# Kernel optimization log

Hardware: AMD Instinct MI355X
Metric: run time of the kernel (lower is better)

The kernel has to match this reference:

```python
import jax, jax.numpy as jnp
import numpy as np

L_XYZ = 10  # fourier freqs for position -> 3 + 6*10 = 63 dims
L_DIR = 4   # fourier freqs for direction -> 3 + 6*4 = 27 dims
DIM = 32    # radiance feature dim per depth layer
PPP = 4     # points (depth layers) per pixel
HID = 128   # MLP hidden width
UCH = 64    # UNet hidden channels


def pe(x, L):
    # fourier positional encoding: [x, sin(2^k x), cos(2^k x)]
    f = (2.0 ** jnp.arange(L)).astype(x.dtype)
    xf = x[..., None] * f  # [..., 3, L]
    s = jnp.sin(xf).reshape(x.shape[:-1] + (-1,))
    c = jnp.cos(xf).reshape(x.shape[:-1] + (-1,))
    return jnp.concatenate([x, s, c], axis=-1)


def conv(x, w, b):
    y = jax.lax.conv_general_dilated(x, w, (1, 1), 'SAME',
                                     dimension_numbers=('NCHW', 'OIHW', 'NCHW'))
    return y + b[None, :, None, None]


def setup_inputs() -> dict:
    key = jax.random.key(0)
    ks = jax.random.split(key, 24)
    H = W = 384
    zbufs = jax.random.uniform(ks[0], (H, W, PPP), dtype=jnp.float32)  # depths in [0,1)
    o = jax.random.normal(ks[1], (H, W, 3), dtype=jnp.float32)
    d = jax.random.normal(ks[2], (H, W, 3), dtype=jnp.float32)
    d = d / jnp.linalg.norm(d, axis=-1, keepdims=True)
    cos = jax.random.uniform(ks[3], (H, W, 1), dtype=jnp.float32) * 0.5 + 0.5
    ray = jnp.concatenate([o, d, cos], axis=-1)  # [H,W,7]
    gt = jax.random.uniform(ks[4], (H, W, 3), dtype=jnp.float32)
    mask_gt = jnp.ones((H, W, 1), dtype=jnp.float32)
    xyz_o = jax.random.normal(ks[5], (1024, 3), dtype=jnp.float32)
    in_xyz = 3 + 6 * L_XYZ
    in_dir = 3 + 6 * L_DIR
    in_ch = DIM * PPP
    p = {}
    p['w1'] = jax.random.normal(ks[6], (in_xyz, HID), dtype=jnp.float32) * 0.05
    p['b1'] = jnp.zeros((HID,), dtype=jnp.float32)
    p['w2'] = jax.random.normal(ks[7], (HID, HID), dtype=jnp.float32) * 0.05
    p['b2'] = jnp.zeros((HID,), dtype=jnp.float32)
    p['w3'] = jax.random.normal(ks[8], (HID + in_dir, DIM), dtype=jnp.float32) * 0.05
    p['b3'] = jnp.zeros((DIM,), dtype=jnp.float32)
    p['mpn_w1'] = jax.random.normal(ks[9], (in_ch, in_ch, 3, 3), dtype=jnp.float32) * 0.02
    p['mpn_b1'] = jnp.zeros((in_ch,), dtype=jnp.float32)
    p['mpn_w2'] = jax.random.normal(ks[10], (in_ch, in_ch, 3, 3), dtype=jnp.float32) * 0.02
    p['mpn_b2'] = jnp.zeros((in_ch,), dtype=jnp.float32)
    p['uw1'] = jax.random.normal(ks[11], (UCH, in_ch, 3, 3), dtype=jnp.float32) * 0.02
    p['ub1'] = jnp.zeros((UCH,), dtype=jnp.float32)
    p['uw2'] = jax.random.normal(ks[12], (UCH, UCH, 3, 3), dtype=jnp.float32) * 0.02
    p['ub2'] = jnp.zeros((UCH,), dtype=jnp.float32)
    p['uw3'] = jax.random.normal(ks[13], (3, UCH, 3, 3), dtype=jnp.float32) * 0.02
    p['ub3'] = jnp.zeros((3,), dtype=jnp.float32)
    inp = {'zbufs': zbufs, 'ray': ray, 'gt': gt, 'mask_gt': mask_gt,
           'isTrain': 1, 'xyz_o': xyz_o}
    inp.update(p)
    return inp


def reference(zbufs, ray, gt, mask_gt, isTrain, xyz_o,
              w1, b1, w2, b2, w3, b3,
              mpn_w1, mpn_b1, mpn_w2, mpn_b2,
              uw1, ub1, uw2, ub2, uw3, ub3):
    H, W, P = zbufs.shape
    o = ray[..., :3]
    dirs = ray[..., 3:6]
    cos = ray[..., 6:7]
    thresh = 0.2 if isTrain else 0.0
    # dense equivalent of boolean-mask gather -> MLP -> scatter into zeros
    mask = (zbufs > thresh).astype(zbufs.dtype)  # [H,W,P]
    # xyz_near = o + dirs * zbuf / cos  (xyznear path)
    xyz = o[..., None, :] + dirs[..., None, :] * zbufs[..., None] / cos[..., None]  # [H,W,P,3]
    x = pe(xyz, L_XYZ)                                   # [H,W,P,63]
    h = jax.nn.relu(x @ w1 + b1)                         # [H,W,P,HID]
    h = jax.nn.relu(h @ w2 + b2)
    dpe = pe(dirs, L_DIR)                                # [H,W,27]
    dpe = jnp.broadcast_to(dpe[..., None, :], h.shape[:-1] + (dpe.shape[-1],))
    feat = jnp.concatenate([h, dpe], axis=-1) @ w3 + b3  # [H,W,P,DIM]
    feat = feat * mask[..., None]                        # zeros where pix_mask is False
    # per-layer permute(2,3,0,1) + cat(dim=1) == [1, P*DIM, H, W]
    rdmp = feat.transpose(2, 3, 0, 1).reshape(1, P * DIM, H, W)
    # MPN: predicted per-channel mask
    m = jax.nn.sigmoid(conv(jax.nn.relu(conv(rdmp, mpn_w1, mpn_b1)), mpn_w2, mpn_b2))
    fuse = rdmp * m
    fea_map = jax.nn.sigmoid(fuse[0, :3].transpose(1, 2, 0))  # [H,W,3]
    # UNet refinement to RGB
    u = jax.nn.relu(conv(fuse, uw1, ub1))
    u = jax.nn.relu(conv(u, uw2, ub2))
    img = jax.nn.sigmoid(conv(u, uw3, ub3))[0].transpose(1, 2, 0)  # [H,W,3]
    return img
```

## Files before the change

kernel.cpp:

```cpp
#include <hip/hip_runtime.h>
#include <hip/hip_bf16.h>
#include <math.h>

typedef __attribute__((ext_vector_type(8))) unsigned short ushort8;
typedef __attribute__((ext_vector_type(8))) __bf16 bf16x8;
typedef __attribute__((ext_vector_type(4))) float floatx4;

constexpr int IMGW = 384;
constexpr int NPIX = IMGW * IMGW;

__device__ __forceinline__ unsigned short f2bf(float f) {
  union { float f; unsigned u; } v; v.f = f;
  unsigned u = v.u;
  return (unsigned short)((u + 0x7fffu + ((u >> 16) & 1u)) >> 16);
}
__device__ __forceinline__ float bf2f(unsigned short h) {
  union { unsigned u; float f; } v; v.u = ((unsigned)h) << 16; return v.f;
}
__device__ __forceinline__ unsigned pk2bf(float a, float b) {
  float2 f2; f2.x = a; f2.y = b;
  __hip_bfloat162 h = __float22bfloat162_rn(f2);
  union { __hip_bfloat162 h; unsigned u; } u; u.h = h; return u.u;
}
__device__ __forceinline__ floatx4 mfma16(bf16x8 a, bf16x8 b, floatx4 c) {
  return __builtin_amdgcn_mfma_f32_16x16x32_bf16(a, b, c, 0, 0, 0);
}
__device__ __forceinline__ bf16x8 lds_frag(const unsigned short* p) {
  return *reinterpret_cast<const bf16x8*>(p);
}
__device__ __forceinline__ bf16x8 u4_to_bf(uint4 v) {
  union { uint4 u; bf16x8 b; } c; c.u = v; return c.b;
}

__device__ __forceinline__ void convB_elem(const float* __restrict__ w,
                                           unsigned short* __restrict__ wt,
                                           int i, int CIN, int G, int NT) {
  int j = i & 7, lane = (i >> 3) & 63;
  int rest = i >> 9;
  int nt = rest % NT; int rest2 = rest / NT;
  int g = rest2 % G;  int ks = rest2 / G;
  int q = lane >> 4, m = lane & 15;
  int co = (g * NT + nt) * 16 + m;
  int k = ks * 32 + q * 8 + j;
  int nb = k / CIN, ci = k - nb * CIN;
  wt[i] = f2bf(w[(co * CIN + ci) * 9 + nb]);
}

__global__ __launch_bounds__(256) void prep_all(
    const float* __restrict__ w1, const float* __restrict__ w2, const float* __restrict__ w3,
    const float* __restrict__ mw1, const float* __restrict__ mw2,
    const float* __restrict__ uw1, const float* __restrict__ uw2,
    unsigned short* __restrict__ w1A, unsigned short* __restrict__ w2A,
    unsigned short* __restrict__ w3A,
    unsigned short* __restrict__ cw1, unsigned short* __restrict__ cw2,
    unsigned short* __restrict__ cu1, unsigned short* __restrict__ cu2) {
  int i = blockIdx.x * 256 + threadIdx.x;
  if (i < 28672) {
    if (i < 8192) {
      int j = i & 7, lane = (i >> 3) & 63, t = i >> 9;
      int mt = t >> 1, ks = t & 1;
      int ch_out = mt * 16 + (lane & 15);
      int kp = ks * 32 + (lane >> 4) * 8 + j;
      int chunk = kp >> 3, sl = kp & 7;
      float val;
      if (chunk == 7 && sl >= 4) {
        int c = sl - 4;
        val = (c < 3) ? w1[c * 128 + ch_out] : 0.0f;
      } else {
        const int coordA[8] = {0,0,0,1,1,2,2,2};
        const int octA[8]   = {0,4,8,2,6,0,4,8};
        const int coordB[8] = {0,0,1,1,1,2,2,2};
        const int octB[8]   = {2,6,0,4,8,2,6,0};
        int rc  = (sl < 4) ? coordA[chunk] : coordB[chunk];
        int oct = ((sl < 4) ? octA[chunk] : octB[chunk]) + ((sl >> 1) & 1);
        int korig = ((sl & 1) ? 33 : 3) + rc * 10 + oct;
        val = w1[korig * 128 + ch_out];
      }
      w1A[i] = f2bf(val);
    } else if (i < 24576) {
      int i2 = i - 8192;
      int j = i2 & 7, lane = (i2 >> 3) & 63, t = i2 >> 9;
      int mt = t >> 2, ks = t & 3;
      int ch_out = mt * 16 + (lane & 15);
      int kp = ks * 32 + (lane >> 4) * 8 + j;
      int c_orig = ((kp >> 2) & 7) * 16 + (kp >> 5) * 4 + (kp & 3);
      w2A[i2] = f2bf(w2[c_orig * 128 + ch_out]);
    } else {
      int i3 = i - 24576;
      int j = i3 & 7, lane = (i3 >> 3) & 63, t = i3 >> 9;
      int mt = t >> 2, ks = t & 3;
      int ch_out = mt * 16 + (lane & 15);
      int kp = ks * 32 + (lane >> 4) * 8 + j;
      int c_orig = ((kp >> 2) & 7) * 16 + (kp >> 5) * 4 + (kp & 3);
      w3A[i3] = f2bf(w3[c_orig * 32 + ch_out]);
    }
    return;
  }
  i -= 28672;
  if (i < 147456) { convB_elem(mw1, cw1, i, 128, 4, 2); return; }
  i -= 147456;
  if (i < 147456) { convB_elem(mw2, cw2, i, 128, 4, 2); return; }
  i -= 147456;
  if (i < 73728)  { convB_elem(uw1, cu1, i, 128, 4, 1); return; }
  i -= 73728;
  if (i < 36864)  { convB_elem(uw2, cu2, i, 64, 4, 1); return; }
}

__global__ __launch_bounds__(256) void dcon_kernel(
    const float* __restrict__ ray, const float* __restrict__ w3,
    const float* __restrict__ b3, float* __restrict__ dconG) {
  int gid = blockIdx.x * 256 + threadIdx.x;
  int pixel = gid >> 5, c = gid & 31;
  const float* r = ray + (size_t)pixel * 7;
  float d0 = r[3], d1 = r[4], d2 = r[5];
  float acc = b3[c];
  acc += d0 * w3[128 * 32 + c] + d1 * w3[129 * 32 + c] + d2 * w3[130 * 32 + c];
  float dv[3] = { d0, d1, d2 };
  #pragma unroll
  for (int cc = 0; cc < 3; ++cc) {
    float fs = 1.0f;
    #pragma unroll
    for (int f = 0; f < 4; ++f) {
      float s, co;
      __sincosf(dv[cc] * fs, &s, &co);
      acc += s * w3[(131 + cc * 4 + f) * 32 + c];
      acc += co * w3[(143 + cc * 4 + f) * 32 + c];
      fs *= 2.0f;
    }
  }
  dconG[gid] = acc;
}

__global__ __launch_bounds__(64, 3) void mlp_kernel(
    const float* __restrict__ zbufs, const float* __restrict__ ray,
    const int* __restrict__ isTrain,
    const float* __restrict__ b1, const float* __restrict__ b2,
    const unsigned short* __restrict__ w1A, const unsigned short* __restrict__ w2A,
    const unsigned short* __restrict__ w3A, const float* __restrict__ dconG,
    unsigned short* __restrict__ rdmp) {
  __shared__ __align__(16) unsigned short H[64 * 136];

  const int lane = threadIdx.x;
  const int q = lane >> 4, m = lane & 15;
  const float thresh = (isTrain[0] != 0) ? 0.2f : 0.0f;

  float fA[2], fB[2];
  int cAi[2], cBi[2];
  #pragma unroll
  for (int half = 0; half < 2; ++half) {
    int ch = half * 4 + q;
    cAi[half] = (ch <= 2) ? 0 : ((ch <= 4) ? 1 : 2);
    fA[half]  = (ch == 0 || ch == 5) ? 1.0f :
                (ch == 1 || ch == 6) ? 16.0f :
                (ch == 2 || ch == 7) ? 256.0f :
                (ch == 3) ? 4.0f : 64.0f;
    cBi[half] = (ch <= 1) ? 0 : ((ch <= 4) ? 1 : 2);
    fB[half]  = (ch == 2) ? 1.0f :
                (ch == 0 || ch == 5) ? 4.0f :
                (ch == 3) ? 16.0f :
                (ch == 1 || ch == 6) ? 64.0f : 256.0f;
  }

  bf16x8 bx[4][2];
  float zs[4];
  #pragma unroll
  for (int nt = 0; nt < 4; ++nt) {
    int s = nt * 16 + m;
    int sg = blockIdx.x * 64 + s;
    int pixel = sg >> 2;
    float z = zbufs[sg];
    zs[nt] = z;
    const float* r = ray + (size_t)pixel * 7;
    float t = z / r[6];
    float xv0 = r[0] + r[3] * t, xv1 = r[1] + r[4] * t, xv2 = r[2] + r[5] * t;
    #pragma unroll
    for (int half = 0; half < 2; ++half) {
      float uA = (cAi[half] == 0) ? xv0 : ((cAi[half] == 1) ? xv1 : xv2);
      float uB = (cBi[half] == 0) ? xv0 : ((cBi[half] == 1) ? xv1 : xv2);
      float sa, ca, sb, cb;
      __sincosf(uA * fA[half], &sa, &ca);
      __sincosf(uB * fB[half], &sb, &cb);
      float t2a = sa + sa;
      float sa1 = t2a * ca, ca1 = fmaf(-t2a, sa, 1.0f);
      float t2b = sb + sb;
      float sb1 = t2b * cb, cb1 = fmaf(-t2b, sb, 1.0f);
      if (half == 1 && q == 3) { sb = xv0; cb = xv1; sb1 = xv2; cb1 = 0.0f; }
      uint4 dv;
      dv.x = pk2bf(sa, ca); dv.y = pk2bf(sa1, ca1);
      dv.z = pk2bf(sb, cb); dv.w = pk2bf(sb1, cb1);
      bx[nt][half] = u4_to_bf(dv);
    }
  }

  #pragma unroll 1
  for (int half = 0; half < 2; ++half) {
    floatx4 acc[4][4];
    #pragma unroll
    for (int mt = 0; mt < 4; ++mt) {
      float4 bb = *reinterpret_cast<const float4*>(b1 + (half * 4 + mt) * 16 + q * 4);
      #pragma unroll
      for (int nt = 0; nt < 4; ++nt) {
        acc[mt][nt][0] = bb.x; acc[mt][nt][1] = bb.y;
        acc[mt][nt][2] = bb.z; acc[mt][nt][3] = bb.w;
      }
    }
    #pragma unroll
    for (int ks = 0; ks < 2; ++ks) {
      #pragma unroll
      for (int mt = 0; mt < 4; ++mt) {
        int mtg = half * 4 + mt;
        bf16x8 a = *reinterpret_cast<const bf16x8*>(w1A + (((mtg << 1) + ks) << 9) + lane * 8);
        #pragma unroll
        for (int nt = 0; nt < 4; ++nt)
          acc[mt][nt] = mfma16(a, bx[nt][ks], acc[mt][nt]);
      }
    }
    #pragma unroll
    for (int nt = 0; nt < 4; ++nt) {
      uint4* base = reinterpret_cast<uint4*>(&H[(nt * 16 + m) * 136 + q * 32 + half * 16]);
      #pragma unroll
      for (int g = 0; g < 2; ++g) {
        uint4 v;
        v.x = pk2bf(fmaxf(acc[2*g][nt][0], 0.0f),   fmaxf(acc[2*g][nt][1], 0.0f));
        v.y = pk2bf(fmaxf(acc[2*g][nt][2], 0.0f),   fmaxf(acc[2*g][nt][3], 0.0f));
        v.z = pk2bf(fmaxf(acc[2*g+1][nt][0], 0.0f), fmaxf(acc[2*g+1][nt][1], 0.0f));
        v.w = pk2bf(fmaxf(acc[2*g+1][nt][2], 0.0f), fmaxf(acc[2*g+1][nt][3], 0.0f));
        base[g] = v;
      }
    }
  }

  {
    uint4 keep[4][2];
    #pragma unroll 1
    for (int half = 0; half < 2; ++half) {
      floatx4 acc[4][4];
      #pragma unroll
      for (int mt = 0; mt < 4; ++mt) {
        float4 bb = *reinterpret_cast<const float4*>(b2 + (half * 4 + mt) * 16 + q * 4);
        #pragma unroll
        for (int nt = 0; nt < 4; ++nt) {
          acc[mt][nt][0] = bb.x; acc[mt][nt][1] = bb.y;
          acc[mt][nt][2] = bb.z; acc[mt][nt][3] = bb.w;
        }
      }
      #pragma unroll 1
      for (int ks = 0; ks < 4; ++ks) {
        bf16x8 bf[4];
        #pragma unroll
        for (int nt = 0; nt < 4; ++nt)
          bf[nt] = lds_frag(H + (nt * 16 + m) * 136 + ks * 32 + q * 8);
        #pragma unroll
        for (int mt = 0; mt < 4; ++mt) {
          int mtg = half * 4 + mt;
          bf16x8 a = *reinterpret_cast<const bf16x8*>(w2A + (((mtg << 2) + ks) << 9) + lane * 8);
          #pragma unroll
          for (int nt = 0; nt < 4; ++nt)
            acc[mt][nt] = mfma16(a, bf[nt], acc[mt][nt]);
        }
      }
      #pragma unroll
      for (int nt = 0; nt < 4; ++nt) {
        #pragma unroll
        for (int g = 0; g < 2; ++g) {
          uint4 v;
          v.x = pk2bf(fmaxf(acc[2*g][nt][0], 0.0f),   fmaxf(acc[2*g][nt][1], 0.0f));
          v.y = pk2bf(fmaxf(acc[2*g][nt][2], 0.0f),   fmaxf(acc[2*g][nt][3], 0.0f));
          v.z = pk2bf(fmaxf(acc[2*g+1][nt][0], 0.0f), fmaxf(acc[2*g+1][nt][1], 0.0f));
          v.w = pk2bf(fmaxf(acc[2*g+1][nt][2], 0.0f), fmaxf(acc[2*g+1][nt][3], 0.0f));
          if (half == 0) {
            keep[nt][g] = v;
          } else {
            *reinterpret_cast<uint4*>(&H[(nt * 16 + m) * 136 + q * 32 + 16 + g * 8]) = v;
          }
        }
      }
    }
    #pragma unroll
    for (int nt = 0; nt < 4; ++nt)
      #pragma unroll
      for (int g = 0; g < 2; ++g)
        *reinterpret_cast<uint4*>(&H[(nt * 16 + m) * 136 + q * 32 + g * 8]) = keep[nt][g];
  }

  {
    floatx4 acc[2][4];
    const float* dg = dconG + (size_t)blockIdx.x * 512;
    #pragma unroll
    for (int nt = 0; nt < 4; ++nt) {
      int s = nt * 16 + m;
      #pragma unroll
      for (int mt = 0; mt < 2; ++mt)
        acc[mt][nt] = *reinterpret_cast<const floatx4*>(dg + (s >> 2) * 32 + mt * 16 + q * 4);
    }
    #pragma unroll 2
    for (int ks = 0; ks < 4; ++ks) {
      bf16x8 bf[4];
      #pragma unroll
      for (int nt = 0; nt < 4; ++nt)
        bf[nt] = lds_frag(H + (nt * 16 + m) * 136 + ks * 32 + q * 8);
      #pragma unroll
      for (int mt = 0; mt < 2; ++mt) {
        bf16x8 a = *reinterpret_cast<const bf16x8*>(w3A + (((mt << 2) + ks) << 9) + lane * 8);
        #pragma unroll
        for (int nt = 0; nt < 4; ++nt)
          acc[mt][nt] = mfma16(a, bf[nt], acc[mt][nt]);
      }
    }
    #pragma unroll
    for (int nt = 0; nt < 4; ++nt) {
      int s = nt * 16 + m;
      float mk = (zs[nt] > thresh) ? 1.0f : 0.0f;
      unsigned short* dst = rdmp + (size_t)blockIdx.x * 2048 + s * 32 + q * 4;
      #pragma unroll
      for (int mt = 0; mt < 2; ++mt) {
        uint2 pk;
        pk.x = pk2bf(acc[mt][nt][0] * mk, acc[mt][nt][1] * mk);
        pk.y = pk2bf(acc[mt][nt][2] * mk, acc[mt][nt][3] * mk);
        *reinterpret_cast<uint2*>(dst + mt * 16) = pk;
      }
    }
  }
}

template<int CIN, int COUT, int MODE, int MINW>
__global__ __launch_bounds__(512, MINW) void conv3x3(
    const unsigned short* __restrict__ in, const unsigned short* __restrict__ wt,
    const float* __restrict__ bias, const unsigned short* __restrict__ rdmp,
    unsigned short* __restrict__ out) {
  constexpr int CP  = CIN + 8;
  constexpr int CH8 = CIN / 8;
  constexpr int KC  = CIN / 32;
  constexpr int NT  = COUT / 64;
  constexpr int GROUPS = KC * 3;
  __shared__ __align__(16) unsigned short lds_in[10 * 18 * CP];

  const int tid = threadIdx.x;
  const int x0 = blockIdx.x * 16, y0 = blockIdx.y * 8;

  for (int i = tid; i < 180 * CH8; i += 512) {
    int pix = i / CH8, part = i - pix * CH8;
    int xx = pix % 18, yy = pix / 18;
    int gx = x0 - 1 + xx, gy = y0 - 1 + yy;
    ushort8 v = {0, 0, 0, 0, 0, 0, 0, 0};
    if (gx >= 0 && gx < IMGW && gy >= 0 && gy < IMGW)
      v = *reinterpret_cast<const ushort8*>(in + ((size_t)(gy * IMGW + gx)) * CIN + part * 8);
    *reinterpret_cast<ushort8*>(&lds_in[pix * CP + part * 8]) = v;
  }
  __syncthreads();

  const int wave = tid >> 6, lane = tid & 63, q = lane >> 4, m = lane & 15;
  const int cw = wave & 3;
  const int rw = wave >> 2;
  floatx4 acc[4][NT] = {};

  auto loadB = [&](int g, bf16x8 (&bb)[3][NT]) {
    int kc = g / 3, dx = g - kc * 3;
    #pragma unroll
    for (int dy = 0; dy < 3; ++dy) {
      int ks = (dy * 3 + dx) * KC + kc;
      #pragma unroll
      for (int nt = 0; nt < NT; ++nt)
        bb[dy][nt] = *reinterpret_cast<const bf16x8*>(
            wt + ((((size_t)ks * 4 + cw) * NT + nt) << 9) + lane * 8);
    }
  };
  auto compute = [&](int g, bf16x8 (&bb)[3][NT]) {
    int kc = g / 3, dx = g - kc * 3;
    bf16x8 a[6];
    #pragma unroll
    for (int rr = 0; rr < 6; ++rr)
      a[rr] = lds_frag(&lds_in[((rw * 4 + rr) * 18 + m + dx) * CP + kc * 32 + q * 8]);
    #pragma unroll
    for (int dy = 0; dy < 3; ++dy)
      #pragma unroll
      for (int nt = 0; nt < NT; ++nt)
        #pragma unroll
        for (int mt = 0; mt < 4; ++mt)
          acc[mt][nt] = mfma16(a[mt + dy], bb[dy][nt], acc[mt][nt]);
  };

  bf16x8 b0[3][NT], b1[3][NT];
  loadB(0, b0);
  #pragma unroll 1
  for (int g = 0; g < GROUPS; g += 2) {
    loadB(g + 1, b1);
    compute(g, b0);
    if (g + 2 < GROUPS) loadB(g + 2, b0);
    compute(g + 1, b1);
  }

  const int co0 = cw * (COUT / 4);
  #pragma unroll
  for (int mt = 0; mt < 4; ++mt) {
    int y = y0 + rw * 4 + mt;
    #pragma unroll
    for (int nt = 0; nt < NT; ++nt) {
      int co = co0 + nt * 16 + m;
      float bb = bias[co];
      #pragma unroll
      for (int r = 0; r < 4; ++r) {
        int pixel = y * IMGW + x0 + q * 4 + r;
        float v = acc[mt][nt][r] + bb;
        if (MODE == 0) {
          v = fmaxf(v, 0.0f);
        } else {
          v = 1.0f / (1.0f + __expf(-v));
          v *= bf2f(rdmp[(size_t)pixel * 128 + co]);
        }
        out[(size_t)pixel * COUT + co] = f2bf(v);
      }
    }
  }
}

__global__ __launch_bounds__(256) void uconv3_kernel(
    const unsigned short* __restrict__ u2, const float* __restrict__ w,
    const float* __restrict__ b, float* __restrict__ out) {
  __shared__ float wl[1728];
  for (int i = threadIdx.x; i < 1728; i += 256) {
    int c = i % 3; int t = i / 3; int ci = t & 63; int nb = t >> 6;
    wl[i] = w[(c * 64 + ci) * 9 + nb];
  }
  __syncthreads();
  int pixel = blockIdx.x * 256 + threadIdx.x;
  int py = pixel / IMGW, px = pixel - py * IMGW;
  float a0 = b[0], a1 = b[1], a2 = b[2];
  for (int nb = 0; nb < 9; ++nb) {
    int gy = py + nb / 3 - 1, gx = px + nb % 3 - 1;
    if (gx < 0 || gx >= IMGW || gy < 0 || gy >= IMGW) continue;
    const unsigned short* src = u2 + (size_t)(gy * IMGW + gx) * 64;
    const float* wp = wl + nb * 192;
    #pragma unroll
    for (int cc = 0; cc < 8; ++cc) {
      ushort8 v = *reinterpret_cast<const ushort8*>(src + cc * 8);
      #pragma unroll
      for (int j = 0; j < 8; ++j) {
        float uv = bf2f(v[j]);
        const float* w3p = wp + (cc * 8 + j) * 3;
        a0 += uv * w3p[0]; a1 += uv * w3p[1]; a2 += uv * w3p[2];
      }
    }
  }
  float* o = out + (size_t)pixel * 3;
  o[0] = 1.0f / (1.0f + __expf(-a0));
  o[1] = 1.0f / (1.0f + __expf(-a1));
  o[2] = 1.0f / (1.0f + __expf(-a2));
}

extern "C" void kernel_launch(void* const* d_in, const int* in_sizes, int n_in,
                              void* d_out, int out_size, void* d_ws, size_t ws_size,
                              hipStream_t stream) {
  (void)in_sizes; (void)n_in; (void)out_size; (void)ws_size;
  const float* zbufs = (const float*)d_in[0];
  const float* ray   = (const float*)d_in[1];
  const int* isTrain = (const int*)d_in[4];
  const float* w1 = (const float*)d_in[6];
  const float* b1 = (const float*)d_in[7];
  const float* w2 = (const float*)d_in[8];
  const float* b2 = (const float*)d_in[9];
  const float* w3 = (const float*)d_in[10];
  const float* b3 = (const float*)d_in[11];
  const float* mpn_w1 = (const float*)d_in[12];
  const float* mpn_b1 = (const float*)d_in[13];
  const float* mpn_w2 = (const float*)d_in[14];
  const float* mpn_b2 = (const float*)d_in[15];
  const float* uw1 = (const float*)d_in[16];
  const float* ub1 = (const float*)d_in[17];
  const float* uw2 = (const float*)d_in[18];
  const float* ub2 = (const float*)d_in[19];
  const float* uw3 = (const float*)d_in[20];
  const float* ub3 = (const float*)d_in[21];
  float* out = (float*)d_out;

  unsigned char* ws = (unsigned char*)d_ws;
  size_t off = 0;
  auto alloc = [&](size_t bytes) -> void* {
    void* p = ws + off; off = (off + bytes + 255) & ~(size_t)255; return p;
  };
  unsigned short* w1A  = (unsigned short*)alloc(8192 * 2);
  unsigned short* w2A  = (unsigned short*)alloc(16384 * 2);
  unsigned short* w3A  = (unsigned short*)alloc(4096 * 2);
  unsigned short* cw1  = (unsigned short*)alloc((size_t)128 * 1152 * 2);
  unsigned short* cw2  = (unsigned short*)alloc((size_t)128 * 1152 * 2);
  unsigned short* cu1  = (unsigned short*)alloc((size_t)64 * 1152 * 2);
  unsigned short* cu2  = (unsigned short*)alloc((size_t)64 * 576 * 2);
  unsigned short* rdmp = (unsigned short*)alloc((size_t)NPIX * 128 * 2);
  unsigned short* t1   = (unsigned short*)alloc((size_t)NPIX * 128 * 2);
  unsigned short* fuse = (unsigned short*)alloc((size_t)NPIX * 128 * 2);
  unsigned short* u1 = t1;
  unsigned short* u2 = rdmp;
  float* dconG = (float*)fuse;

  prep_all<<<1696, 256, 0, stream>>>(w1, w2, w3, mpn_w1, mpn_w2, uw1, uw2,
                                     w1A, w2A, w3A, cw1, cw2, cu1, cu2);
  dcon_kernel<<<NPIX * 32 / 256, 256, 0, stream>>>(ray, w3, b3, dconG);
  mlp_kernel<<<NPIX * 4 / 64, 64, 0, stream>>>(zbufs, ray, isTrain, b1, b2,
                                               w1A, w2A, w3A, dconG, rdmp);

  dim3 cgrid(IMGW / 16, IMGW / 8);
  conv3x3<128, 128, 0, 4><<<cgrid, 512, 0, stream>>>(rdmp, cw1, mpn_b1, nullptr, t1);
  conv3x3<128, 128, 1, 4><<<cgrid, 512, 0, stream>>>(t1, cw2, mpn_b2, rdmp, fuse);
  conv3x3<128, 64, 0, 4><<<cgrid, 512, 0, stream>>>(fuse, cu1, ub1, nullptr, u1);
  conv3x3<64, 64, 0, 4><<<cgrid, 512, 0, stream>>>(u1, cu2, ub2, nullptr, u2);
  uconv3_kernel<<<NPIX / 256, 256, 0, stream>>>(u2, uw3, ub3, out);
}
```

Baseline: 337.3 us.

## Split MLP kernel output halves across two waves per block

The MLP kernel now launches 128 threads per block. Each of the two waves handles one half of the hidden/output channels for the same 64 samples, where before a single wave looped over both halves serially. Barriers are added around the shared hidden-activation buffer so layer-2 outputs are written only after both waves finish reading layer-1 results. This doubles the waves working on each sample tile and aims for more latency hiding. The cost is that both waves redundantly compute the positional encoding, and the extra barriers add synchronisation overhead.

```diff
diff --git a/kernel.cpp b/kernel.cpp
--- a/kernel.cpp
+++ b/kernel.cpp
@@ -131,7 +131,7 @@
   dconG[gid] = acc;
 }
 
-__global__ __launch_bounds__(64, 3) void mlp_kernel(
+__global__ __launch_bounds__(128, 4) void mlp_kernel(
     const float* __restrict__ zbufs, const float* __restrict__ ray,
     const int* __restrict__ isTrain,
     const float* __restrict__ b1, const float* __restrict__ b2,
@@ -140,25 +140,27 @@
     unsigned short* __restrict__ rdmp) {
   __shared__ __align__(16) unsigned short H[64 * 136];
 
-  const int lane = threadIdx.x;
+  const int tid = threadIdx.x;
+  const int half = tid >> 6;
+  const int lane = tid & 63;
   const int q = lane >> 4, m = lane & 15;
   const float thresh = (isTrain[0] != 0) ? 0.2f : 0.0f;
 
   float fA[2], fB[2];
   int cAi[2], cBi[2];
   #pragma unroll
-  for (int half = 0; half < 2; ++half) {
-    int ch = half * 4 + q;
-    cAi[half] = (ch <= 2) ? 0 : ((ch <= 4) ? 1 : 2);
-    fA[half]  = (ch == 0 || ch == 5) ? 1.0f :
-                (ch == 1 || ch == 6) ? 16.0f :
-                (ch == 2 || ch == 7) ? 256.0f :
-                (ch == 3) ? 4.0f : 64.0f;
-    cBi[half] = (ch <= 1) ? 0 : ((ch <= 4) ? 1 : 2);
-    fB[half]  = (ch == 2) ? 1.0f :
-                (ch == 0 || ch == 5) ? 4.0f :
-                (ch == 3) ? 16.0f :
-                (ch == 1 || ch == 6) ? 64.0f : 256.0f;
+  for (int ks = 0; ks < 2; ++ks) {
+    int ch = ks * 4 + q;
+    cAi[ks] = (ch <= 2) ? 0 : ((ch <= 4) ? 1 : 2);
+    fA[ks]  = (ch == 0 || ch == 5) ? 1.0f :
+              (ch == 1 || ch == 6) ? 16.0f :
+              (ch == 2 || ch == 7) ? 256.0f :
+              (ch == 3) ? 4.0f : 64.0f;
+    cBi[ks] = (ch <= 1) ? 0 : ((ch <= 4) ? 1 : 2);
+    fB[ks]  = (ch == 2) ? 1.0f :
+              (ch == 0 || ch == 5) ? 4.0f :
+              (ch == 3) ? 16.0f :
+              (ch == 1 || ch == 6) ? 64.0f : 256.0f;
   }
 
   bf16x8 bx[4][2];
@@ -174,26 +176,25 @@
     float t = z / r[6];
     float xv0 = r[0] + r[3] * t, xv1 = r[1] + r[4] * t, xv2 = r[2] + r[5] * t;
     #pragma unroll
-    for (int half = 0; half < 2; ++half) {
-      float uA = (cAi[half] == 0) ? xv0 : ((cAi[half] == 1) ? xv1 : xv2);
-      float uB = (cBi[half] == 0) ? xv0 : ((cBi[half] == 1) ? xv1 : xv2);
+    for (int ks = 0; ks < 2; ++ks) {
+      float uA = (cAi[ks] == 0) ? xv0 : ((cAi[ks] == 1) ? xv1 : xv2);
+      float uB = (cBi[ks] == 0) ? xv0 : ((cBi[ks] == 1) ? xv1 : xv2);
       float sa, ca, sb, cb;
-      __sincosf(uA * fA[half], &sa, &ca);
-      __sincosf(uB * fB[half], &sb, &cb);
+      __sincosf(uA * fA[ks], &sa, &ca);
+      __sincosf(uB * fB[ks], &sb, &cb);
       float t2a = sa + sa;
       float sa1 = t2a * ca, ca1 = fmaf(-t2a, sa, 1.0f);
       float t2b = sb + sb;
       float sb1 = t2b * cb, cb1 = fmaf(-t2b, sb, 1.0f);
-      if (half == 1 && q == 3) { sb = xv0; cb = xv1; sb1 = xv2; cb1 = 0.0f; }
+      if (ks == 1 && q == 3) { sb = xv0; cb = xv1; sb1 = xv2; cb1 = 0.0f; }
       uint4 dv;
       dv.x = pk2bf(sa, ca); dv.y = pk2bf(sa1, ca1);
       dv.z = pk2bf(sb, cb); dv.w = pk2bf(sb1, cb1);
-      bx[nt][half] = u4_to_bf(dv);
-    }
-  }
-
-  #pragma unroll 1
-  for (int half = 0; half < 2; ++half) {
+      bx[nt][ks] = u4_to_bf(dv);
+    }
+  }
+
+  {
     floatx4 acc[4][4];
     #pragma unroll
     for (int mt = 0; mt < 4; ++mt) {
@@ -229,11 +230,11 @@
       }
     }
   }
+  __syncthreads();
 
   {
     uint4 keep[4][2];
-    #pragma unroll 1
-    for (int half = 0; half < 2; ++half) {
+    {
       floatx4 acc[4][4];
       #pragma unroll
       for (int mt = 0; mt < 4; ++mt) {
@@ -268,30 +269,26 @@
           v.y = pk2bf(fmaxf(acc[2*g][nt][2], 0.0f),   fmaxf(acc[2*g][nt][3], 0.0f));
           v.z = pk2bf(fmaxf(acc[2*g+1][nt][0], 0.0f), fmaxf(acc[2*g+1][nt][1], 0.0f));
           v.w = pk2bf(fmaxf(acc[2*g+1][nt][2], 0.0f), fmaxf(acc[2*g+1][nt][3], 0.0f));
-          if (half == 0) {
-            keep[nt][g] = v;
-          } else {
-            *reinterpret_cast<uint4*>(&H[(nt * 16 + m) * 136 + q * 32 + 16 + g * 8]) = v;
-          }
+          keep[nt][g] = v;
         }
       }
     }
+    __syncthreads();
     #pragma unroll
     for (int nt = 0; nt < 4; ++nt)
       #pragma unroll
       for (int g = 0; g < 2; ++g)
-        *reinterpret_cast<uint4*>(&H[(nt * 16 + m) * 136 + q * 32 + g * 8]) = keep[nt][g];
-  }
+        *reinterpret_cast<uint4*>(&H[(nt * 16 + m) * 136 + q * 32 + half * 16 + g * 8]) = keep[nt][g];
+  }
+  __syncthreads();
 
   {
-    floatx4 acc[2][4];
+    floatx4 acc[4];
     const float* dg = dconG + (size_t)blockIdx.x * 512;
     #pragma unroll
     for (int nt = 0; nt < 4; ++nt) {
       int s = nt * 16 + m;
-      #pragma unroll
-      for (int mt = 0; mt < 2; ++mt)
-        acc[mt][nt] = *reinterpret_cast<const floatx4*>(dg + (s >> 2) * 32 + mt * 16 + q * 4);
+      acc[nt] = *reinterpret_cast<const floatx4*>(dg + (s >> 2) * 32 + half * 16 + q * 4);
     }
     #pragma unroll 2
     for (int ks = 0; ks < 4; ++ks) {
@@ -299,26 +296,20 @@
       #pragma unroll
       for (int nt = 0; nt < 4; ++nt)
         bf[nt] = lds_frag(H + (nt * 16 + m) * 136 + ks * 32 + q * 8);
-      #pragma unroll
-      for (int mt = 0; mt < 2; ++mt) {
-        bf16x8 a = *reinterpret_cast<const bf16x8*>(w3A + (((mt << 2) + ks) << 9) + lane * 8);
-        #pragma unroll
-        for (int nt = 0; nt < 4; ++nt)
-          acc[mt][nt] = mfma16(a, bf[nt], acc[mt][nt]);
-      }
+      bf16x8 a = *reinterpret_cast<const bf16x8*>(w3A + (((half << 2) + ks) << 9) + lane * 8);
+      #pragma unroll
+      for (int nt = 0; nt < 4; ++nt)
+        acc[nt] = mfma16(a, bf[nt], acc[nt]);
     }
     #pragma unroll
     for (int nt = 0; nt < 4; ++nt) {
       int s = nt * 16 + m;
       float mk = (zs[nt] > thresh) ? 1.0f : 0.0f;
-      unsigned short* dst = rdmp + (size_t)blockIdx.x * 2048 + s * 32 + q * 4;
-      #pragma unroll
-      for (int mt = 0; mt < 2; ++mt) {
-        uint2 pk;
-        pk.x = pk2bf(acc[mt][nt][0] * mk, acc[mt][nt][1] * mk);
-        pk.y = pk2bf(acc[mt][nt][2] * mk, acc[mt][nt][3] * mk);
-        *reinterpret_cast<uint2*>(dst + mt * 16) = pk;
-      }
+      unsigned short* dst = rdmp + (size_t)blockIdx.x * 2048 + s * 32 + q * 4 + half * 16;
+      uint2 pk;
+      pk.x = pk2bf(acc[nt][0] * mk, acc[nt][1] * mk);
+      pk.y = pk2bf(acc[nt][2] * mk, acc[nt][3] * mk);
+      *reinterpret_cast<uint2*>(dst) = pk;
     }
   }
 }
@@ -495,8 +486,8 @@
   prep_all<<<1696, 256, 0, stream>>>(w1, w2, w3, mpn_w1, mpn_w2, uw1, uw2,
                                      w1A, w2A, w3A, cw1, cw2, cu1, cu2);
   dcon_kernel<<<NPIX * 32 / 256, 256, 0, stream>>>(ray, w3, b3, dconG);
-  mlp_kernel<<<NPIX * 4 / 64, 64, 0, stream>>>(zbufs, ray, isTrain, b1, b2,
-                                               w1A, w2A, w3A, dconG, rdmp);
+  mlp_kernel<<<NPIX * 4 / 64, 128, 0, stream>>>(zbufs, ray, isTrain, b1, b2,
+                                                w1A, w2A, w3A, dconG, rdmp);
 
   dim3 cgrid(IMGW / 16, IMGW / 8);
   conv3x3<128, 128, 0, 4><<<cgrid, 512, 0, stream>>>(rdmp, cw1, mpn_b1, nullptr, t1);
```

Result: slower. 354.7 us (+5.2%).
